# Optimization experiments

Hardware: AMD Instinct MI355X
Metric: run time of the kernel (lower is better)

Reference implementation:

```python
import jax, jax.numpy as jnp
import numpy as np

BETA = 0.99
THRESHOLD = 1.0
RESET = 0.8
A_POS = 0.005
A_NEG = 0.005
TRACE_DECAY = 0.9
W_CLAMP = 0.1

B, I, O = 512, 4096, 4096


def setup_inputs() -> dict:
    key = jax.random.key(0)
    k1, k2, k3, k4, k5 = jax.random.split(key, 5)
    in_spikes = (jax.random.uniform(k1, (B, I)) < 0.1).astype(jnp.float32)
    # nn.Linear default init: U(-1/sqrt(in), 1/sqrt(in))
    bound = 1.0 / np.sqrt(I)
    weight = jax.random.uniform(k2, (O, I), minval=-bound, maxval=bound, dtype=jnp.float32)
    membrane = jax.random.uniform(k3, (B, O), dtype=jnp.float32) * 0.5
    trace_pre = jax.random.uniform(k4, (B, I), dtype=jnp.float32) * 0.3
    trace_post = jax.random.uniform(k5, (B, O), dtype=jnp.float32) * 0.3
    return {"in_spikes": in_spikes, "weight": weight, "membrane": membrane,
            "trace_pre": trace_pre, "trace_post": trace_post}


def reference(in_spikes, weight, membrane, trace_pre, trace_post):
    # weighted input: [B, O]
    weighted = jnp.matmul(in_spikes, weight.T)
    # LIF neuron update
    mem = membrane * BETA + weighted
    spikes = (mem > THRESHOLD).astype(jnp.float32)
    new_membrane = jnp.where(spikes > 0, mem - RESET, mem)
    # STDP trace update
    tp = trace_pre * TRACE_DECAY + in_spikes        # [B, I]
    tq = trace_post * TRACE_DECAY + spikes          # [B, O]
    # torch: (tq[:,None,:]*a_pos*tp[:,:,None] - tp[:,:,None]*a_neg*tq[:,None,:]).sum(0).T
    # == (a_pos - a_neg) * tq.T @ tp  -> [O, I]; rank-B GEMM, no [B,I,O] intermediate
    dw = (A_POS - A_NEG) * jnp.einsum('bo,bi->oi', tq, tp)
    new_weight = jnp.clip(weight + dw, -W_CLAMP, W_CLAMP)
    return spikes, new_membrane, new_weight, tp, tq
```

## Files before the change

### kernel.cpp

```cpp
#include <hip/hip_runtime.h>
#include <stdint.h>
#include <stddef.h>


#define I_DIM 4096
#define K2 8192

typedef _Float16 f16x8 __attribute__((ext_vector_type(8)));
typedef float    f32x4 __attribute__((ext_vector_type(4)));

#define OUT_SPIKES 0
#define OUT_NEWMEM 2097152
#define OUT_NEWW   4194304
#define OUT_TP     20971520
#define OUT_TQ     23068672

#define WS_A2   0u
#define WS_B2   8388608u
#define WS_PART 75497472u

__device__ __forceinline__ void async16(void* lds, const void* g) {
  __builtin_amdgcn_global_load_lds((__attribute__((address_space(1))) const void*)g,
                                   (__attribute__((address_space(3))) void*)lds, 16, 0, 0);
}

__global__ __launch_bounds__(256) void prep_weight_kernel(
    const float* __restrict__ w, float* __restrict__ outw, _Float16* __restrict__ b2) {
  const size_t i = (size_t)blockIdx.x * 256 + threadIdx.x;
  const size_t f = i * 8;
  const int o = (int)(f >> 12);
  const int c = (int)(f & 4095);
  const f32x4* w4 = (const f32x4*)(w + f);
  f32x4 x0 = w4[0], x1 = w4[1];
  *(f32x4*)(outw + f) = x0;
  *(f32x4*)(outw + f + 4) = x1;
  f16x8 hi, lo;
#pragma unroll
  for (int k = 0; k < 4; ++k) {
    _Float16 h0 = (_Float16)x0[k];
    hi[k] = h0;
    lo[k] = (_Float16)((x0[k] - (float)h0) * 1024.0f);
    _Float16 h1 = (_Float16)x1[k];
    hi[k + 4] = h1;
    lo[k + 4] = (_Float16)((x1[k] - (float)h1) * 1024.0f);
  }
  _Float16* row = b2 + (size_t)o * K2 + c;
  *(f16x8*)row = hi;
  *(f16x8*)(row + 4096) = lo;
}

__global__ __launch_bounds__(256) void prep_spikes_kernel(
    const float* __restrict__ sp, const float* __restrict__ tpre,
    float* __restrict__ tp_out, _Float16* __restrict__ a2) {
  const size_t i = (size_t)blockIdx.x * 256 + threadIdx.x;
  const size_t f = i * 8;
  const int b = (int)(f >> 12);
  const int c = (int)(f & 4095);
  const f32x4* s4 = (const f32x4*)(sp + f);
  const f32x4* p4 = (const f32x4*)(tpre + f);
  f32x4 s0 = s4[0], s1 = s4[1];
  f32x4 t0 = p4[0], t1 = p4[1];
  f32x4 r0, r1;
  f16x8 h, hs;
#pragma unroll
  for (int k = 0; k < 4; ++k) {
    r0[k] = t0[k] * 0.9f + s0[k];
    r1[k] = t1[k] * 0.9f + s1[k];
    h[k] = (_Float16)s0[k];
    h[k + 4] = (_Float16)s1[k];
    hs[k] = (_Float16)(s0[k] * 0.0009765625f);
    hs[k + 4] = (_Float16)(s1[k] * 0.0009765625f);
  }
  *(f32x4*)(tp_out + f) = r0;
  *(f32x4*)(tp_out + f + 4) = r1;
  _Float16* row = a2 + (size_t)b * K2 + c;
  *(f16x8*)row = h;
  *(f16x8*)(row + 4096) = hs;
}

__global__ __launch_bounds__(256, 2) void gemm_split_kernel(
    const _Float16* __restrict__ a2, const _Float16* __restrict__ b2,
    float* __restrict__ part) {
  __shared__ __align__(16) char smem[65536];
  const int tid = threadIdx.x;
  const int l = tid & 63;
  const int w = tid >> 6;

  const int bid = blockIdx.x;
  const int x = bid & 7;
  const int j = bid >> 3;
  const int m = j & 3;
  const int g = (j >> 2) * 8 + x;
  const int s = g >> 5;
  const int n = g & 31;

  const int bm0 = m * 128;
  const int bn0 = n * 128;
  const int kbase = s * 2048;
  const int wm = w >> 1;
  const int wn = w & 1;

  const _Float16* Ap = a2 + (size_t)bm0 * K2 + kbase;
  const _Float16* Bp = b2 + (size_t)bn0 * K2 + kbase;

  auto stage = [&](char* base, int k0) {
#pragma unroll
    for (int q = 0; q < 4; ++q) {
      const int c = q * 256 + tid;
      const int row = c >> 3;
      const int col8 = ((c & 7) ^ (row & 7)) * 8;
      async16(base + c * 16, Ap + (size_t)row * K2 + k0 + col8);
    }
#pragma unroll
    for (int q = 0; q < 4; ++q) {
      const int c = q * 256 + tid;
      const int row = c >> 3;
      const int col8 = ((c & 7) ^ (row & 7)) * 8;
      async16(base + 16384 + c * 16, Bp + (size_t)row * K2 + k0 + col8);
    }
  };

  f32x4 acc[4][4];
  const f32x4 zero = {0.0f, 0.0f, 0.0f, 0.0f};
#pragma unroll
  for (int a = 0; a < 4; ++a)
#pragma unroll
    for (int b = 0; b < 4; ++b) acc[a][b] = zero;

  const int swz = (l & 7) << 4;
  const int koff = (l >> 4) << 4;
  const int lrow = l & 15;
  int rowA[4], rowB[4];
#pragma unroll
  for (int ff = 0; ff < 4; ++ff) {
    rowA[ff] = (wm * 64 + ff * 16 + lrow) * 128;
    rowB[ff] = 16384 + (wn * 64 + ff * 16 + lrow) * 128;
  }

  stage(smem, 0);
  __syncthreads();

  for (int t = 0; t < 32; ++t) {
    char* cur = smem + ((t & 1) << 15);
    if (t < 31) stage(smem + ((~t & 1) << 15), (t + 1) * 64);
#pragma unroll
    for (int kf = 0; kf < 2; ++kf) {
      const int cb = (kf * 64 + koff) ^ swz;
      f16x8 af[4], bf[4];
#pragma unroll
      for (int ff = 0; ff < 4; ++ff) af[ff] = *(const f16x8*)(cur + rowA[ff] + cb);
#pragma unroll
      for (int ff = 0; ff < 4; ++ff) bf[ff] = *(const f16x8*)(cur + rowB[ff] + cb);
#pragma unroll
      for (int mf = 0; mf < 4; ++mf)
#pragma unroll
        for (int nf = 0; nf < 4; ++nf)
          acc[mf][nf] = __builtin_amdgcn_mfma_f32_16x16x32_f16(af[mf], bf[nf], acc[mf][nf], 0, 0, 0);
    }
    __syncthreads();
  }

  float* P = part + (size_t)s * 2097152;
#pragma unroll
  for (int mf = 0; mf < 4; ++mf) {
    const int pr0 = bm0 + wm * 64 + mf * 16 + ((l >> 4) << 2);
#pragma unroll
    for (int nf = 0; nf < 4; ++nf) {
      const int pc = bn0 + wn * 64 + nf * 16 + lrow;
#pragma unroll
      for (int jj = 0; jj < 4; ++jj)
        P[(size_t)(pr0 + jj) * 4096 + pc] = acc[mf][nf][jj];
    }
  }
}

__global__ __launch_bounds__(256) void reduce_lif_kernel(
    const float* __restrict__ part, const float* __restrict__ membrane,
    const float* __restrict__ tpost, float* __restrict__ out) {
  const size_t i = (size_t)blockIdx.x * 256 + threadIdx.x;
  const f32x4* p4 = (const f32x4*)part;
  f32x4 sum = p4[i];
#pragma unroll
  for (int k = 1; k < 4; ++k) {
    f32x4 v = p4[(size_t)k * 524288 + i];
#pragma unroll
    for (int jj = 0; jj < 4; ++jj) sum[jj] += v[jj];
  }
  f32x4 mm = ((const f32x4*)membrane)[i];
  f32x4 tq0 = ((const f32x4*)tpost)[i];
  f32x4 spk, nmem, tqo;
#pragma unroll
  for (int jj = 0; jj < 4; ++jj) {
    const float mem = mm[jj] * 0.99f + sum[jj];
    const float sp = (mem > 1.0f) ? 1.0f : 0.0f;
    spk[jj] = sp;
    nmem[jj] = (mem > 1.0f) ? (mem - 0.8f) : mem;
    tqo[jj] = tq0[jj] * 0.9f + sp;
  }
  ((f32x4*)(out + OUT_SPIKES))[i] = spk;
  ((f32x4*)(out + OUT_NEWMEM))[i] = nmem;
  ((f32x4*)(out + OUT_TQ))[i] = tqo;
}

extern "C" void kernel_launch(void* const* d_in, const int* in_sizes, int n_in,
                              void* d_out, int out_size, void* d_ws, size_t ws_size,
                              hipStream_t stream) {
  const float* in_spikes  = (const float*)d_in[0];
  const float* weight     = (const float*)d_in[1];
  const float* membrane   = (const float*)d_in[2];
  const float* trace_pre  = (const float*)d_in[3];
  const float* trace_post = (const float*)d_in[4];
  float* out = (float*)d_out;
  char* ws = (char*)d_ws;
  _Float16* a2 = (_Float16*)(ws + WS_A2);
  _Float16* b2 = (_Float16*)(ws + WS_B2);
  float* part = (float*)(ws + WS_PART);

  prep_weight_kernel<<<8192, 256, 0, stream>>>(weight, out + OUT_NEWW, b2);
  prep_spikes_kernel<<<1024, 256, 0, stream>>>(in_spikes, trace_pre, out + OUT_TP, a2);
  gemm_split_kernel<<<512, 256, 0, stream>>>(a2, b2, part);
  reduce_lif_kernel<<<2048, 256, 0, stream>>>(part, membrane, trace_post, out);
}
```

Baseline: 234.8 us.

## Fuse split-K reduction and LIF update into GEMM via last-block atomic counter

The GEMM moves from 4-way to 8-way split-K, giving 1024 blocks. It drops LDS double buffering, halving shared memory so three blocks fit per CU. The separate reduce/LIF kernel is removed: the last block to finish each output tile, found with an atomic counter that prep_spikes zeroes, sums the partials and applies the LIF and trace update. This saves a kernel launch and raises occupancy, but load/compute overlap within a block is lost, partial-buffer traffic doubles, and the tile-finishing blocks run a serialized tail reduction.

```diff
diff --git a/kernel.cpp b/kernel.cpp
--- a/kernel.cpp
+++ b/kernel.cpp
@@ -18,6 +18,7 @@
 #define WS_A2   0u
 #define WS_B2   8388608u
 #define WS_PART 75497472u
+#define WS_CNT  142606336u
 
 __device__ __forceinline__ void async16(void* lds, const void* g) {
   __builtin_amdgcn_global_load_lds((__attribute__((address_space(1))) const void*)g,
@@ -51,7 +52,8 @@
 
 __global__ __launch_bounds__(256) void prep_spikes_kernel(
     const float* __restrict__ sp, const float* __restrict__ tpre,
-    float* __restrict__ tp_out, _Float16* __restrict__ a2) {
+    float* __restrict__ tp_out, _Float16* __restrict__ a2, int* __restrict__ cnt) {
+  if (blockIdx.x == 0 && threadIdx.x < 128) cnt[threadIdx.x] = 0;
   const size_t i = (size_t)blockIdx.x * 256 + threadIdx.x;
   const size_t f = i * 8;
   const int b = (int)(f >> 12);
@@ -78,79 +80,66 @@
   *(f16x8*)(row + 4096) = hs;
 }
 
-__global__ __launch_bounds__(256, 2) void gemm_split_kernel(
+__global__ __launch_bounds__(256, 3) void gemm_fused_kernel(
     const _Float16* __restrict__ a2, const _Float16* __restrict__ b2,
-    float* __restrict__ part) {
-  __shared__ __align__(16) char smem[65536];
+    const float* __restrict__ membrane, const float* __restrict__ tpost,
+    float* __restrict__ part, int* __restrict__ cnt, float* __restrict__ out) {
+  __shared__ __align__(16) char smem[32768];
+  __shared__ int s_last;
   const int tid = threadIdx.x;
   const int l = tid & 63;
   const int w = tid >> 6;
 
   const int bid = blockIdx.x;
-  const int x = bid & 7;
-  const int j = bid >> 3;
-  const int m = j & 3;
-  const int g = (j >> 2) * 8 + x;
-  const int s = g >> 5;
-  const int n = g & 31;
-
+  const int s = bid & 7;
+  const int idx = bid >> 3;
+  const int m = idx & 3;
+  const int n = idx >> 2;
   const int bm0 = m * 128;
   const int bn0 = n * 128;
-  const int kbase = s * 2048;
+  const int kbase = s * 1024;
   const int wm = w >> 1;
   const int wn = w & 1;
 
   const _Float16* Ap = a2 + (size_t)bm0 * K2 + kbase;
   const _Float16* Bp = b2 + (size_t)bn0 * K2 + kbase;
 
-  auto stage = [&](char* base, int k0) {
+  f32x4 acc[4][4];
+  const f32x4 zero = {0.0f, 0.0f, 0.0f, 0.0f};
+#pragma unroll
+  for (int a = 0; a < 4; ++a)
+#pragma unroll
+    for (int b_ = 0; b_ < 4; ++b_) acc[a][b_] = zero;
+
+  const int swz = (l & 7) << 4;
+  const int koff = (l >> 4) << 4;
+  const int lrow = l & 15;
+  int rowA[4], rowB[4];
+#pragma unroll
+  for (int ff = 0; ff < 4; ++ff) {
+    rowA[ff] = (wm * 64 + ff * 16 + lrow) * 128;
+    rowB[ff] = 16384 + (wn * 64 + ff * 16 + lrow) * 128;
+  }
+
+  for (int t = 0; t < 16; ++t) {
+    const int k0 = t * 64;
 #pragma unroll
     for (int q = 0; q < 4; ++q) {
       const int c = q * 256 + tid;
       const int row = c >> 3;
       const int col8 = ((c & 7) ^ (row & 7)) * 8;
-      async16(base + c * 16, Ap + (size_t)row * K2 + k0 + col8);
-    }
-#pragma unroll
-    for (int q = 0; q < 4; ++q) {
-      const int c = q * 256 + tid;
-      const int row = c >> 3;
-      const int col8 = ((c & 7) ^ (row & 7)) * 8;
-      async16(base + 16384 + c * 16, Bp + (size_t)row * K2 + k0 + col8);
-    }
-  };
-
-  f32x4 acc[4][4];
-  const f32x4 zero = {0.0f, 0.0f, 0.0f, 0.0f};
-#pragma unroll
-  for (int a = 0; a < 4; ++a)
-#pragma unroll
-    for (int b = 0; b < 4; ++b) acc[a][b] = zero;
-
-  const int swz = (l & 7) << 4;
-  const int koff = (l >> 4) << 4;
-  const int lrow = l & 15;
-  int rowA[4], rowB[4];
-#pragma unroll
-  for (int ff = 0; ff < 4; ++ff) {
-    rowA[ff] = (wm * 64 + ff * 16 + lrow) * 128;
-    rowB[ff] = 16384 + (wn * 64 + ff * 16 + lrow) * 128;
-  }
-
-  stage(smem, 0);
-  __syncthreads();
-
-  for (int t = 0; t < 32; ++t) {
-    char* cur = smem + ((t & 1) << 15);
-    if (t < 31) stage(smem + ((~t & 1) << 15), (t + 1) * 64);
+      async16(smem + c * 16, Ap + (size_t)row * K2 + k0 + col8);
+      async16(smem + 16384 + c * 16, Bp + (size_t)row * K2 + k0 + col8);
+    }
+    __syncthreads();
 #pragma unroll
     for (int kf = 0; kf < 2; ++kf) {
       const int cb = (kf * 64 + koff) ^ swz;
       f16x8 af[4], bf[4];
 #pragma unroll
-      for (int ff = 0; ff < 4; ++ff) af[ff] = *(const f16x8*)(cur + rowA[ff] + cb);
-#pragma unroll
-      for (int ff = 0; ff < 4; ++ff) bf[ff] = *(const f16x8*)(cur + rowB[ff] + cb);
+      for (int ff = 0; ff < 4; ++ff) af[ff] = *(const f16x8*)(smem + rowA[ff] + cb);
+#pragma unroll
+      for (int ff = 0; ff < 4; ++ff) bf[ff] = *(const f16x8*)(smem + rowB[ff] + cb);
 #pragma unroll
       for (int mf = 0; mf < 4; ++mf)
 #pragma unroll
@@ -172,34 +161,49 @@
         P[(size_t)(pr0 + jj) * 4096 + pc] = acc[mf][nf][jj];
     }
   }
-}
-
-__global__ __launch_bounds__(256) void reduce_lif_kernel(
-    const float* __restrict__ part, const float* __restrict__ membrane,
-    const float* __restrict__ tpost, float* __restrict__ out) {
-  const size_t i = (size_t)blockIdx.x * 256 + threadIdx.x;
+
+  __syncthreads();
+  if (tid == 0) {
+    __threadfence();
+    int old = __hip_atomic_fetch_add(&cnt[idx], 1, __ATOMIC_ACQ_REL, __HIP_MEMORY_SCOPE_AGENT);
+    s_last = (old == 7);
+  }
+  __syncthreads();
+  if (!s_last) return;
+  __threadfence();
+
   const f32x4* p4 = (const f32x4*)part;
-  f32x4 sum = p4[i];
-#pragma unroll
-  for (int k = 1; k < 4; ++k) {
-    f32x4 v = p4[(size_t)k * 524288 + i];
-#pragma unroll
-    for (int jj = 0; jj < 4; ++jj) sum[jj] += v[jj];
-  }
-  f32x4 mm = ((const f32x4*)membrane)[i];
-  f32x4 tq0 = ((const f32x4*)tpost)[i];
-  f32x4 spk, nmem, tqo;
-#pragma unroll
-  for (int jj = 0; jj < 4; ++jj) {
-    const float mem = mm[jj] * 0.99f + sum[jj];
-    const float sp = (mem > 1.0f) ? 1.0f : 0.0f;
-    spk[jj] = sp;
-    nmem[jj] = (mem > 1.0f) ? (mem - 0.8f) : mem;
-    tqo[jj] = tq0[jj] * 0.9f + sp;
-  }
-  ((f32x4*)(out + OUT_SPIKES))[i] = spk;
-  ((f32x4*)(out + OUT_NEWMEM))[i] = nmem;
-  ((f32x4*)(out + OUT_TQ))[i] = tqo;
+  const f32x4* mm4 = (const f32x4*)membrane;
+  const f32x4* tq4 = (const f32x4*)tpost;
+  f32x4* sp4 = (f32x4*)(out + OUT_SPIKES);
+  f32x4* nm4 = (f32x4*)(out + OUT_NEWMEM);
+  f32x4* to4 = (f32x4*)(out + OUT_TQ);
+#pragma unroll
+  for (int k = 0; k < 16; ++k) {
+    const int v = tid + 256 * k;
+    const int r = bm0 + (v >> 5);
+    const size_t off = (size_t)r * 1024 + (bn0 >> 2) + (v & 31);
+    f32x4 sum = p4[off];
+#pragma unroll
+    for (int sp = 1; sp < 8; ++sp) {
+      f32x4 pv = p4[(size_t)sp * 524288 + off];
+#pragma unroll
+      for (int jj = 0; jj < 4; ++jj) sum[jj] += pv[jj];
+    }
+    f32x4 mb = mm4[off], tb = tq4[off];
+    f32x4 spk, nmem, tqo;
+#pragma unroll
+    for (int jj = 0; jj < 4; ++jj) {
+      const float mem = mb[jj] * 0.99f + sum[jj];
+      const float spike = (mem > 1.0f) ? 1.0f : 0.0f;
+      spk[jj] = spike;
+      nmem[jj] = (mem > 1.0f) ? (mem - 0.8f) : mem;
+      tqo[jj] = tb[jj] * 0.9f + spike;
+    }
+    sp4[off] = spk;
+    nm4[off] = nmem;
+    to4[off] = tqo;
+  }
 }
 
 extern "C" void kernel_launch(void* const* d_in, const int* in_sizes, int n_in,
@@ -215,9 +219,9 @@
   _Float16* a2 = (_Float16*)(ws + WS_A2);
   _Float16* b2 = (_Float16*)(ws + WS_B2);
   float* part = (float*)(ws + WS_PART);
+  int* cnt = (int*)(ws + WS_CNT);
 
   prep_weight_kernel<<<8192, 256, 0, stream>>>(weight, out + OUT_NEWW, b2);
-  prep_spikes_kernel<<<1024, 256, 0, stream>>>(in_spikes, trace_pre, out + OUT_TP, a2);
-  gemm_split_kernel<<<512, 256, 0, stream>>>(a2, b2, part);
-  reduce_lif_kernel<<<2048, 256, 0, stream>>>(part, membrane, trace_post, out);
-}
+  prep_spikes_kernel<<<1024, 256, 0, stream>>>(in_spikes, trace_pre, out + OUT_TP, a2, cnt);
+  gemm_fused_kernel<<<1024, 256, 0, stream>>>(a2, b2, membrane, trace_post, part, cnt, out);
+}
```

Result: slower. 418.0 us (+78.0%).
